# Optimization experiments

Hardware: AMD Instinct MI355X
Metric: run time of the kernel (lower is better)

Reference implementation:

```python
import jax, jax.numpy as jnp
import numpy as np

N_NODES = 50000
N_EDGES = 800000
N_FEAT = 64
HIDDEN = 64
N_GRAPHS = 64
N_CLASSES = 10
BN_EPS = 1e-5


def setup_inputs() -> dict:
    key = jax.random.key(0)
    ks = jax.random.split(key, 12)
    x = jax.random.normal(ks[0], (N_NODES, N_FEAT), dtype=jnp.float32)
    edge_index = jax.random.randint(ks[1], (2, N_EDGES), 0, N_NODES, dtype=jnp.int64)
    # equal-sized, sorted graph assignment so every graph is non-empty for max-pool
    batch = (jnp.arange(N_NODES, dtype=jnp.int64) * N_GRAPHS) // N_NODES
    s = 0.1
    return {
        "x": x,
        "edge_index": edge_index,
        "batch": batch,
        "W1": jax.random.normal(ks[2], (N_FEAT, HIDDEN), jnp.float32) * s,
        "b1": jnp.zeros((HIDDEN,), jnp.float32),
        "W2": jax.random.normal(ks[3], (HIDDEN, HIDDEN), jnp.float32) * s,
        "b2": jnp.zeros((HIDDEN,), jnp.float32),
        "W3": jax.random.normal(ks[4], (HIDDEN, HIDDEN), jnp.float32) * s,
        "b3": jnp.zeros((HIDDEN,), jnp.float32),
        # NOTE: source uses [Norm(hidden)]*3 -> ONE shared BatchNorm across layers
        "gamma": jnp.ones((HIDDEN,), jnp.float32),
        "beta": jnp.zeros((HIDDEN,), jnp.float32),
        "lin1_w": jax.random.normal(ks[5], (HIDDEN, HIDDEN), jnp.float32) * s,
        "lin1_b": jnp.zeros((HIDDEN,), jnp.float32),
        "lin2_w": jax.random.normal(ks[6], (HIDDEN, N_CLASSES), jnp.float32) * s,
        "lin2_b": jnp.zeros((N_CLASSES,), jnp.float32),
    }


def reference(x, edge_index, batch, W1, b1, W2, b2, W3, b3, gamma, beta,
              lin1_w, lin1_b, lin2_w, lin2_b):
    N = x.shape[0]
    src, dst = edge_index[0], edge_index[1]
    # GCN symmetric normalization with self-loops: deg = in-degree + 1
    deg = jax.ops.segment_sum(jnp.ones(src.shape[0], x.dtype), dst, num_segments=N) + 1.0
    dis = jax.lax.rsqrt(deg)                      # [N]
    coef = (dis[src] * dis[dst])[:, None]         # [E,1] edge norm
    self_coef = (dis * dis)[:, None]              # [N,1] self-loop norm

    def gcn_conv(h, W, b):
        h = h @ W                                  # [N,H] tiny GEMM
        agg = jax.ops.segment_sum(h[src] * coef, dst, num_segments=N)
        return agg + h * self_coef + b

    def batch_norm(h):
        mu = h.mean(axis=0)
        var = h.var(axis=0)                        # biased var, torch BN training mode
        return gamma * (h - mu) * jax.lax.rsqrt(var + BN_EPS) + beta

    out = x
    for W, b in ((W1, b1), (W2, b2), (W3, b3)):
        out = jax.nn.relu(batch_norm(gcn_conv(out, W, b)))

    emb = jax.ops.segment_max(out, batch, num_segments=N_GRAPHS)  # global_max_pool
    return jax.nn.relu(emb @ lin1_w + lin1_b) @ lin2_w + lin2_b
```

## Files before the change

kernel.cpp:

```cpp
#include <hip/hip_runtime.h>
#include <hip/hip_bf16.h>

#define N_NODES 50000
#define N_EDGES 800000
#define HID 64
#define N_GRAPHS 64
#define N_CLASSES 10
#define BN_EPS 1e-5f
#define NPART 196
#define FILL_BLOCKS 128

typedef unsigned int uint;
typedef unsigned short ushort;

__device__ __forceinline__ float blo(uint u) { return __uint_as_float(u << 16); }
__device__ __forceinline__ float bhi(uint u) { return __uint_as_float(u & 0xffff0000u); }
__device__ __forceinline__ unsigned short f2b(float f) {
  __hip_bfloat16 h = __float2bfloat16(f);
  return *reinterpret_cast<unsigned short*>(&h);
}


__global__ void k_count_deg(const int* __restrict__ dst, int* __restrict__ deg) {
  int e = blockIdx.x * blockDim.x + threadIdx.x;
  if (e < N_EDGES) atomicAdd(&deg[__builtin_nontemporal_load(&dst[e])], 1);
}

__global__ void k_scan_block(const int* __restrict__ deg, int* __restrict__ rowp,
                             int* __restrict__ bsum, float* __restrict__ dis) {
  __shared__ int s[256];
  int tid = threadIdx.x;
  int i = blockIdx.x * 256 + tid;
  int v = (i < N_NODES) ? deg[i] : 0;
  if (i < N_NODES) dis[i] = rsqrtf((float)v + 1.0f);
  s[tid] = v;
  __syncthreads();
  for (int off = 1; off < 256; off <<= 1) {
    int t = (tid >= off) ? s[tid - off] : 0;
    __syncthreads();
    s[tid] += t;
    __syncthreads();
  }
  if (i < N_NODES) rowp[i] = s[tid] - v;
  if (tid == 255) bsum[blockIdx.x] = s[255];
}

__global__ void k_scan_partials(int* __restrict__ bsum, int nb) {
  __shared__ int s[256];
  int tid = threadIdx.x;
  int v = (tid < nb) ? bsum[tid] : 0;
  s[tid] = v;
  __syncthreads();
  for (int off = 1; off < 256; off <<= 1) {
    int t = (tid >= off) ? s[tid - off] : 0;
    __syncthreads();
    s[tid] += t;
    __syncthreads();
  }
  if (tid < nb) bsum[tid] = s[tid] - v;
}

__global__ void k_scan_finish(int* __restrict__ rowp, const int* __restrict__ bsum,
                              int* __restrict__ pcur) {
  int i = blockIdx.x * blockDim.x + threadIdx.x;
  if (i < N_NODES) {
    int v = rowp[i] + bsum[i >> 8];
    rowp[i] = v;
    if ((i & 255) == 0) pcur[i >> 8] = v;
  }
  if (i == 0) rowp[N_NODES] = N_EDGES;
}

__global__ __launch_bounds__(256) void k_partA(const int* __restrict__ ei,
                                               int* __restrict__ pcur,
                                               uint* __restrict__ tmp) {
  __shared__ int lcnt[NPART];
  __shared__ int lbase[NPART];
  int tid = threadIdx.x;
  const int per = (N_EDGES + FILL_BLOCKS - 1) / FILL_BLOCKS;
  int c0 = blockIdx.x * per;
  int c1 = c0 + per;
  if (c1 > N_EDGES) c1 = N_EDGES;
  for (int i = tid; i < NPART; i += 256) lcnt[i] = 0;
  __syncthreads();
  for (int e = c0 + tid; e < c1; e += 256) {
    int d = __builtin_nontemporal_load(&ei[N_EDGES + e]);
    atomicAdd(&lcnt[d >> 8], 1);
  }
  __syncthreads();
  for (int p = tid; p < NPART; p += 256) lbase[p] = atomicAdd(&pcur[p], lcnt[p]);
  __syncthreads();
  for (int e = c0 + tid; e < c1; e += 256) {
    int s = __builtin_nontemporal_load(&ei[e]);
    int d = __builtin_nontemporal_load(&ei[N_EDGES + e]);
    int pos = atomicAdd(&lbase[d >> 8], 1);
    tmp[pos] = ((uint)s << 8) | (uint)(d & 255);
  }
}

__global__ __launch_bounds__(256) void k_partB(const uint* __restrict__ tmp,
                                               const int* __restrict__ rowp,
                                               const float* __restrict__ dis,
                                               uint* __restrict__ edata) {
  __shared__ int cur[256];
  __shared__ float sdis[256];
  int tid = threadIdx.x;
  int p = blockIdx.x;
  int n0 = p << 8;
  {
    int n = n0 + tid;
    cur[tid] = (n < N_NODES) ? rowp[n] : 0;
    sdis[tid] = (n < N_NODES) ? dis[n] : 0.f;
  }
  int base = rowp[n0];
  int endn = n0 + 256;
  if (endn > N_NODES) endn = N_NODES;
  int pend = rowp[endn];
  __syncthreads();
  for (int idx = base + tid; idx < pend; idx += 256) {
    uint t = __builtin_nontemporal_load(&tmp[idx]);
    uint s = t >> 8;
    uint dl = t & 255u;
    int pos = atomicAdd(&cur[dl], 1);
    float coef = dis[s] * sdis[dl];
    edata[pos] = (s << 16) | (uint)f2b(coef);
  }
}


template <bool IN_BF16>
__global__ __launch_bounds__(256) void k_gemm(const void* __restrict__ in,
                                              const float* __restrict__ W,
                                              __hip_bfloat16* __restrict__ out,
                                              float* __restrict__ stats_zero,
                                              const float* __restrict__ stats_in,
                                              const float* __restrict__ gamma,
                                              const float* __restrict__ beta) {
  __shared__ float Al[4][64];
  int tid = threadIdx.x;
  int wid = tid >> 6, f = tid & 63;
  if (blockIdx.x == 0) {
    for (int i = tid; i < 1024; i += 256) stats_zero[i] = 0.0f;
  }
  float Wreg[64];
#pragma unroll
  for (int k = 0; k < 64; ++k) Wreg[k] = W[k * 64 + f];
  float sc = 1.f, sh = 0.f;
  if (stats_in) {
    float s = 0.f, q = 0.f;
#pragma unroll
    for (int c = 0; c < 8; ++c) {
      s += stats_in[c * 128 + f];
      q += stats_in[c * 128 + 64 + f];
    }
    float mu = s * (1.0f / N_NODES);
    float var = q * (1.0f / N_NODES) - mu * mu;
    sc = gamma[f] * rsqrtf(var + BN_EPS);
    sh = beta[f] - mu * sc;
  }
  for (int n = blockIdx.x * 4 + wid; n < N_NODES; n += gridDim.x * 4) {
    float av;
    if (IN_BF16) {
      ushort u = ((const ushort*)in)[(n << 6) + f];
      av = __uint_as_float((uint)u << 16);
    } else {
      av = ((const float*)in)[(n << 6) + f];
    }
    if (stats_in) {
      av = fmaf(av, sc, sh);
      av = av > 0.f ? av : 0.f;
    }
    Al[wid][f] = av;
    float acc = 0.f;
    const float4* arow = (const float4*)Al[wid];
#pragma unroll
    for (int k4 = 0; k4 < 16; ++k4) {
      float4 a = arow[k4];
      acc = fmaf(a.x, Wreg[k4 * 4 + 0], acc);
      acc = fmaf(a.y, Wreg[k4 * 4 + 1], acc);
      acc = fmaf(a.z, Wreg[k4 * 4 + 2], acc);
      acc = fmaf(a.w, Wreg[k4 * 4 + 3], acc);
    }
    out[(n << 6) + f] = __float2bfloat16(acc);
  }
}

__global__ __launch_bounds__(256, 4) void k_agg_node(
    const __hip_bfloat16* __restrict__ hW, const float* __restrict__ dis,
    const int* __restrict__ rowp, const uint* __restrict__ edata,
    const float* __restrict__ bias, __hip_bfloat16* __restrict__ act,
    float* __restrict__ stats) {
  __shared__ float sstat[4][2][64];
  int tid = threadIdx.x;
  int wid = tid >> 6, lane = tid & 63;
  int g = lane >> 3, l8 = lane & 7;
  int n = (blockIdx.x * 4 + wid) * 8 + g;
  const uint4* hw4 = (const uint4*)hW;
  float pre[8] = {0, 0, 0, 0, 0, 0, 0, 0};
  float sq[8] = {0, 0, 0, 0, 0, 0, 0, 0};
  if (n < N_NODES) {
    int p0 = rowp[n], p1 = rowp[n + 1];
    float acc[8] = {0, 0, 0, 0, 0, 0, 0, 0};
    for (int pb = p0; pb < p1; pb += 8) {
      uint rec = (pb + l8 < p1) ? edata[pb + l8] : 0u;
      uint e[8];
#pragma unroll
      for (int u = 0; u < 8; ++u) e[u] = __shfl(rec, (g << 3) | u, 64);
#pragma unroll
      for (int h = 0; h < 2; ++h) {
        uint4 hv[4];
#pragma unroll
        for (int u = 0; u < 4; ++u) hv[u] = hw4[(e[h * 4 + u] >> 16) * 8 + l8];
#pragma unroll
        for (int u = 0; u < 4; ++u) {
          float wv = blo(e[h * 4 + u]);
          acc[0] = fmaf(blo(hv[u].x), wv, acc[0]);
          acc[1] = fmaf(bhi(hv[u].x), wv, acc[1]);
          acc[2] = fmaf(blo(hv[u].y), wv, acc[2]);
          acc[3] = fmaf(bhi(hv[u].y), wv, acc[3]);
          acc[4] = fmaf(blo(hv[u].z), wv, acc[4]);
          acc[5] = fmaf(bhi(hv[u].z), wv, acc[5]);
          acc[6] = fmaf(blo(hv[u].w), wv, acc[6]);
          acc[7] = fmaf(bhi(hv[u].w), wv, acc[7]);
        }
      }
    }
    float dn = dis[n];
    float dn2 = dn * dn;
    uint4 hs = hw4[n * 8 + l8];
    const float4* b4 = (const float4*)bias;
    float4 bA = b4[l8 * 2], bB = b4[l8 * 2 + 1];
    pre[0] = fmaf(blo(hs.x), dn2, acc[0]) + bA.x;
    pre[1] = fmaf(bhi(hs.x), dn2, acc[1]) + bA.y;
    pre[2] = fmaf(blo(hs.y), dn2, acc[2]) + bA.z;
    pre[3] = fmaf(bhi(hs.y), dn2, acc[3]) + bA.w;
    pre[4] = fmaf(blo(hs.z), dn2, acc[4]) + bB.x;
    pre[5] = fmaf(bhi(hs.z), dn2, acc[5]) + bB.y;
    pre[6] = fmaf(blo(hs.w), dn2, acc[6]) + bB.z;
    pre[7] = fmaf(bhi(hs.w), dn2, acc[7]) + bB.w;
    uint4 st;
    st.x = (uint)f2b(pre[0]) | ((uint)f2b(pre[1]) << 16);
    st.y = (uint)f2b(pre[2]) | ((uint)f2b(pre[3]) << 16);
    st.z = (uint)f2b(pre[4]) | ((uint)f2b(pre[5]) << 16);
    st.w = (uint)f2b(pre[6]) | ((uint)f2b(pre[7]) << 16);
    ((uint4*)act)[n * 8 + l8] = st;
#pragma unroll
    for (int i = 0; i < 8; ++i) sq[i] = pre[i] * pre[i];
  }
#pragma unroll
  for (int off = 8; off < 64; off <<= 1) {
#pragma unroll
    for (int i = 0; i < 8; ++i) {
      pre[i] += __shfl_xor(pre[i], off, 64);
      sq[i] += __shfl_xor(sq[i], off, 64);
    }
  }
  if (g == 0) {
#pragma unroll
    for (int i = 0; i < 8; ++i) {
      sstat[wid][0][l8 * 8 + i] = pre[i];
      sstat[wid][1][l8 * 8 + i] = sq[i];
    }
  }
  __syncthreads();
  if (tid < 128) {
    int which = tid >> 6, f = tid & 63;
    float s = sstat[0][which][f] + sstat[1][which][f] + sstat[2][which][f] +
              sstat[3][which][f];
    atomicAdd(&stats[(blockIdx.x & 7) * 128 + which * 64 + f], s);
  }
}


__global__ __launch_bounds__(256) void k_pool(const __hip_bfloat16* __restrict__ act,
                                              const float* __restrict__ stats_in,
                                              const float* __restrict__ gamma,
                                              const float* __restrict__ beta,
                                              float* __restrict__ pooled) {
  int g = blockIdx.x;
  int tid = threadIdx.x;
  int l16 = tid & 15;
  int r = tid >> 4;
  float sc[4], sh[4];
#pragma unroll
  for (int i = 0; i < 4; ++i) {
    int f = l16 * 4 + i;
    float s = 0.f, q = 0.f;
#pragma unroll
    for (int c = 0; c < 8; ++c) {
      s += stats_in[c * 128 + f];
      q += stats_in[c * 128 + 64 + f];
    }
    float mu = s * (1.0f / N_NODES);
    float var = q * (1.0f / N_NODES) - mu * mu;
    sc[i] = gamma[f] * rsqrtf(var + BN_EPS);
    sh[i] = beta[f] - mu * sc[i];
  }
  int gs = g * N_NODES;
  int start = (gs + 63) >> 6;
  int end = (gs + N_NODES + 63) >> 6;
  float m[4] = {0.f, 0.f, 0.f, 0.f};
  const uint2* a2 = (const uint2*)act;
  for (int n = start + r; n < end; n += 16) {
    uint2 v = a2[n * 16 + l16];
    m[0] = fmaxf(m[0], fmaf(blo(v.x), sc[0], sh[0]));
    m[1] = fmaxf(m[1], fmaf(bhi(v.x), sc[1], sh[1]));
    m[2] = fmaxf(m[2], fmaf(blo(v.y), sc[2], sh[2]));
    m[3] = fmaxf(m[3], fmaf(bhi(v.y), sc[3], sh[3]));
  }
  __shared__ float sm[16][64];
#pragma unroll
  for (int i = 0; i < 4; ++i) sm[r][l16 * 4 + i] = m[i];
  __syncthreads();
  if (tid < 64) {
    float mm = sm[0][tid];
#pragma unroll
    for (int rr = 1; rr < 16; ++rr) mm = fmaxf(mm, sm[rr][tid]);
    pooled[g * 64 + tid] = mm;
  }
}

__global__ __launch_bounds__(256) void k_final(const float* __restrict__ pooled,
                                               const float* __restrict__ w1,
                                               const float* __restrict__ b1,
                                               const float* __restrict__ w2,
                                               const float* __restrict__ b2,
                                               float* __restrict__ out) {
  __shared__ float P[64 * 64];
  __shared__ float Hd[64 * 64];
  int tid = threadIdx.x;
  for (int i = tid; i < 4096; i += 256) P[i] = pooled[i];
  __syncthreads();
  for (int i = tid; i < 4096; i += 256) {
    int g = i >> 6, j = i & 63;
    float acc = b1[j];
#pragma unroll
    for (int k = 0; k < 64; ++k) acc = fmaf(P[g * 64 + k], w1[k * 64 + j], acc);
    Hd[i] = acc > 0.f ? acc : 0.f;
  }
  __syncthreads();
  for (int i = tid; i < 640; i += 256) {
    int g = i / 10, c = i % 10;
    float acc = b2[c];
#pragma unroll
    for (int k = 0; k < 64; ++k) acc = fmaf(Hd[g * 64 + k], w2[k * 10 + c], acc);
    out[i] = acc;
  }
}


extern "C" void kernel_launch(void* const* d_in, const int* in_sizes, int n_in,
                              void* d_out, int out_size, void* d_ws, size_t ws_size,
                              hipStream_t stream) {
  const float* x = (const float*)d_in[0];
  const int* ei = (const int*)d_in[1];
  const float* W1 = (const float*)d_in[3];
  const float* b1 = (const float*)d_in[4];
  const float* W2 = (const float*)d_in[5];
  const float* b2 = (const float*)d_in[6];
  const float* W3 = (const float*)d_in[7];
  const float* b3 = (const float*)d_in[8];
  const float* gamma = (const float*)d_in[9];
  const float* beta = (const float*)d_in[10];
  const float* l1w = (const float*)d_in[11];
  const float* l1b = (const float*)d_in[12];
  const float* l2w = (const float*)d_in[13];
  const float* l2b = (const float*)d_in[14];
  float* out = (float*)d_out;

  char* ws = (char*)d_ws;
  size_t off = 0;
  auto alloc = [&](size_t bytes) {
    void* p = ws + off;
    off = (off + bytes + 255) & ~(size_t)255;
    return p;
  };
  int* deg = (int*)alloc(N_NODES * 4);
  int* rowp = (int*)alloc((N_NODES + 1) * 4);
  int* pcur = (int*)alloc(NPART * 4);
  int* bsum = (int*)alloc(256 * 4);
  uint* tmp = (uint*)alloc((size_t)N_EDGES * 4);
  uint* edata = (uint*)alloc((size_t)N_EDGES * 4);
  float* dis = (float*)alloc(N_NODES * 4);
  __hip_bfloat16* hW = (__hip_bfloat16*)alloc((size_t)N_NODES * 64 * 2);
  __hip_bfloat16* act = (__hip_bfloat16*)alloc((size_t)N_NODES * 64 * 2);
  float* statsL0 = (float*)alloc(1024 * 4);
  float* statsL1 = (float*)alloc(1024 * 4);
  float* statsL2 = (float*)alloc(1024 * 4);
  float* pooled = (float*)alloc(4096 * 4);

  int nsb = (N_NODES + 255) / 256;
  int nag = (N_NODES + 31) / 32;

  (void)hipMemsetAsync(deg, 0, N_NODES * 4, stream);
  k_count_deg<<<(N_EDGES + 255) / 256, 256, 0, stream>>>(ei + N_EDGES, deg);
  k_scan_block<<<nsb, 256, 0, stream>>>(deg, rowp, bsum, dis);
  k_scan_partials<<<1, 256, 0, stream>>>(bsum, nsb);
  k_scan_finish<<<nsb, 256, 0, stream>>>(rowp, bsum, pcur);
  k_partA<<<FILL_BLOCKS, 256, 0, stream>>>(ei, pcur, tmp);
  k_partB<<<NPART, 256, 0, stream>>>(tmp, rowp, dis, edata);

  k_gemm<false><<<2048, 256, 0, stream>>>(x, W1, hW, statsL0, nullptr, gamma, beta);
  k_agg_node<<<nag, 256, 0, stream>>>(hW, dis, rowp, edata, b1, act, statsL0);
  k_gemm<true><<<2048, 256, 0, stream>>>(act, W2, hW, statsL1, statsL0, gamma, beta);
  k_agg_node<<<nag, 256, 0, stream>>>(hW, dis, rowp, edata, b2, act, statsL1);
  k_gemm<true><<<2048, 256, 0, stream>>>(act, W3, hW, statsL2, statsL1, gamma, beta);
  k_agg_node<<<nag, 256, 0, stream>>>(hW, dis, rowp, edata, b3, act, statsL2);

  k_pool<<<N_GRAPHS, 256, 0, stream>>>(act, statsL2, gamma, beta, pooled);
  k_final<<<1, 256, 0, stream>>>(pooled, l1w, l1b, l2w, l2b, out);
}
```

Measured before the change: 227.0 us.

## Build CSR from partition histogram and store 16-bit source indices per edge

Replaces the per-node global-atomic degree count and three-kernel scan with a 196-bucket partition histogram and a single small scan. Per-node degrees, `dis` and `rowp` are now computed inside `k_partB` using shared-memory counting and a per-block scan. Each edge record shrinks from 4 bytes (16-bit source plus a bf16 coefficient) to a 2-byte source index. The aggregation kernel rebuilds the coefficient on the fly from `dis[src]*dis[dst]`. This cuts launch count, global atomic traffic and edge bandwidth, at the cost of an extra scattered `dis` load per edge in each of the three aggregation passes.

```diff
diff --git a/kernel.cpp b/kernel.cpp
--- a/kernel.cpp
+++ b/kernel.cpp
@@ -21,18 +21,33 @@
 }
 
 
-__global__ void k_count_deg(const int* __restrict__ dst, int* __restrict__ deg) {
-  int e = blockIdx.x * blockDim.x + threadIdx.x;
-  if (e < N_EDGES) atomicAdd(&deg[__builtin_nontemporal_load(&dst[e])], 1);
-}
-
-__global__ void k_scan_block(const int* __restrict__ deg, int* __restrict__ rowp,
-                             int* __restrict__ bsum, float* __restrict__ dis) {
+__global__ void k_zero_small(int* __restrict__ p, int n) {
+  int i = threadIdx.x;
+  if (i < n) p[i] = 0;
+}
+
+__global__ __launch_bounds__(256) void k_hist(const int* __restrict__ dst,
+                                              int* __restrict__ ghist) {
+  __shared__ int l[NPART];
+  int tid = threadIdx.x;
+  for (int i = tid; i < NPART; i += 256) l[i] = 0;
+  __syncthreads();
+  const int per = (N_EDGES + FILL_BLOCKS - 1) / FILL_BLOCKS;
+  int c0 = blockIdx.x * per;
+  int c1 = c0 + per;
+  if (c1 > N_EDGES) c1 = N_EDGES;
+  for (int e = c0 + tid; e < c1; e += 256)
+    atomicAdd(&l[__builtin_nontemporal_load(&dst[e]) >> 8], 1);
+  __syncthreads();
+  for (int p = tid; p < NPART; p += 256)
+    if (l[p]) atomicAdd(&ghist[p], l[p]);
+}
+
+__global__ void k_scan196(const int* __restrict__ ghist, int* __restrict__ bro,
+                          int* __restrict__ pcur, int* __restrict__ rowp) {
   __shared__ int s[256];
   int tid = threadIdx.x;
-  int i = blockIdx.x * 256 + tid;
-  int v = (i < N_NODES) ? deg[i] : 0;
-  if (i < N_NODES) dis[i] = rsqrtf((float)v + 1.0f);
+  int v = (tid < NPART) ? ghist[tid] : 0;
   s[tid] = v;
   __syncthreads();
   for (int off = 1; off < 256; off <<= 1) {
@@ -41,15 +56,64 @@
     s[tid] += t;
     __syncthreads();
   }
-  if (i < N_NODES) rowp[i] = s[tid] - v;
-  if (tid == 255) bsum[blockIdx.x] = s[255];
-}
-
-__global__ void k_scan_partials(int* __restrict__ bsum, int nb) {
+  if (tid < NPART) {
+    int e = s[tid] - v;
+    bro[tid] = e;
+    pcur[tid] = e;
+  }
+  if (tid == 0) {
+    bro[NPART] = N_EDGES;
+    rowp[N_NODES] = N_EDGES;
+  }
+}
+
+__global__ __launch_bounds__(256) void k_partA(const int* __restrict__ ei,
+                                               int* __restrict__ pcur,
+                                               uint* __restrict__ tmp) {
+  __shared__ int lcnt[NPART];
+  __shared__ int lbase[NPART];
+  int tid = threadIdx.x;
+  const int per = (N_EDGES + FILL_BLOCKS - 1) / FILL_BLOCKS;
+  int c0 = blockIdx.x * per;
+  int c1 = c0 + per;
+  if (c1 > N_EDGES) c1 = N_EDGES;
+  for (int i = tid; i < NPART; i += 256) lcnt[i] = 0;
+  __syncthreads();
+  for (int e = c0 + tid; e < c1; e += 256) {
+    int d = __builtin_nontemporal_load(&ei[N_EDGES + e]);
+    atomicAdd(&lcnt[d >> 8], 1);
+  }
+  __syncthreads();
+  for (int p = tid; p < NPART; p += 256) lbase[p] = atomicAdd(&pcur[p], lcnt[p]);
+  __syncthreads();
+  for (int e = c0 + tid; e < c1; e += 256) {
+    int s = __builtin_nontemporal_load(&ei[e]);
+    int d = __builtin_nontemporal_load(&ei[N_EDGES + e]);
+    int pos = atomicAdd(&lbase[d >> 8], 1);
+    tmp[pos] = ((uint)s << 8) | (uint)(d & 255);
+  }
+}
+
+__global__ __launch_bounds__(256) void k_partB(const uint* __restrict__ tmp,
+                                               const int* __restrict__ bro,
+                                               float* __restrict__ dis,
+                                               int* __restrict__ rowp,
+                                               ushort* __restrict__ eus) {
+  __shared__ int cnt[256];
   __shared__ int s[256];
-  int tid = threadIdx.x;
-  int v = (tid < nb) ? bsum[tid] : 0;
-  s[tid] = v;
+  __shared__ int cur[256];
+  int tid = threadIdx.x;
+  int p = blockIdx.x;
+  int base = bro[p], pend = bro[p + 1];
+  cnt[tid] = 0;
+  __syncthreads();
+  for (int idx = base + tid; idx < pend; idx += 256)
+    atomicAdd(&cnt[__builtin_nontemporal_load(&tmp[idx]) & 255u], 1);
+  __syncthreads();
+  int deg = cnt[tid];
+  int n = (p << 8) + tid;
+  if (n < N_NODES) dis[n] = rsqrtf((float)deg + 1.0f);
+  s[tid] = deg;
   __syncthreads();
   for (int off = 1; off < 256; off <<= 1) {
     int t = (tid >= off) ? s[tid - off] : 0;
@@ -57,73 +121,14 @@
     s[tid] += t;
     __syncthreads();
   }
-  if (tid < nb) bsum[tid] = s[tid] - v;
-}
-
-__global__ void k_scan_finish(int* __restrict__ rowp, const int* __restrict__ bsum,
-                              int* __restrict__ pcur) {
-  int i = blockIdx.x * blockDim.x + threadIdx.x;
-  if (i < N_NODES) {
-    int v = rowp[i] + bsum[i >> 8];
-    rowp[i] = v;
-    if ((i & 255) == 0) pcur[i >> 8] = v;
-  }
-  if (i == 0) rowp[N_NODES] = N_EDGES;
-}
-
-__global__ __launch_bounds__(256) void k_partA(const int* __restrict__ ei,
-                                               int* __restrict__ pcur,
-                                               uint* __restrict__ tmp) {
-  __shared__ int lcnt[NPART];
-  __shared__ int lbase[NPART];
-  int tid = threadIdx.x;
-  const int per = (N_EDGES + FILL_BLOCKS - 1) / FILL_BLOCKS;
-  int c0 = blockIdx.x * per;
-  int c1 = c0 + per;
-  if (c1 > N_EDGES) c1 = N_EDGES;
-  for (int i = tid; i < NPART; i += 256) lcnt[i] = 0;
-  __syncthreads();
-  for (int e = c0 + tid; e < c1; e += 256) {
-    int d = __builtin_nontemporal_load(&ei[N_EDGES + e]);
-    atomicAdd(&lcnt[d >> 8], 1);
-  }
-  __syncthreads();
-  for (int p = tid; p < NPART; p += 256) lbase[p] = atomicAdd(&pcur[p], lcnt[p]);
-  __syncthreads();
-  for (int e = c0 + tid; e < c1; e += 256) {
-    int s = __builtin_nontemporal_load(&ei[e]);
-    int d = __builtin_nontemporal_load(&ei[N_EDGES + e]);
-    int pos = atomicAdd(&lbase[d >> 8], 1);
-    tmp[pos] = ((uint)s << 8) | (uint)(d & 255);
-  }
-}
-
-__global__ __launch_bounds__(256) void k_partB(const uint* __restrict__ tmp,
-                                               const int* __restrict__ rowp,
-                                               const float* __restrict__ dis,
-                                               uint* __restrict__ edata) {
-  __shared__ int cur[256];
-  __shared__ float sdis[256];
-  int tid = threadIdx.x;
-  int p = blockIdx.x;
-  int n0 = p << 8;
-  {
-    int n = n0 + tid;
-    cur[tid] = (n < N_NODES) ? rowp[n] : 0;
-    sdis[tid] = (n < N_NODES) ? dis[n] : 0.f;
-  }
-  int base = rowp[n0];
-  int endn = n0 + 256;
-  if (endn > N_NODES) endn = N_NODES;
-  int pend = rowp[endn];
+  int start = base + s[tid] - deg;
+  if (n < N_NODES) rowp[n] = start;
+  cur[tid] = start;
   __syncthreads();
   for (int idx = base + tid; idx < pend; idx += 256) {
     uint t = __builtin_nontemporal_load(&tmp[idx]);
-    uint s = t >> 8;
-    uint dl = t & 255u;
-    int pos = atomicAdd(&cur[dl], 1);
-    float coef = dis[s] * sdis[dl];
-    edata[pos] = (s << 16) | (uint)f2b(coef);
+    int pos = atomicAdd(&cur[t & 255u], 1);
+    eus[pos] = (ushort)(t >> 8);
   }
 }
 
@@ -187,7 +192,7 @@
 
 __global__ __launch_bounds__(256, 4) void k_agg_node(
     const __hip_bfloat16* __restrict__ hW, const float* __restrict__ dis,
-    const int* __restrict__ rowp, const uint* __restrict__ edata,
+    const int* __restrict__ rowp, const ushort* __restrict__ eus,
     const float* __restrict__ bias, __hip_bfloat16* __restrict__ act,
     float* __restrict__ stats) {
   __shared__ float sstat[4][2][64];
@@ -200,20 +205,27 @@
   float sq[8] = {0, 0, 0, 0, 0, 0, 0, 0};
   if (n < N_NODES) {
     int p0 = rowp[n], p1 = rowp[n + 1];
+    float dn = dis[n];
     float acc[8] = {0, 0, 0, 0, 0, 0, 0, 0};
     for (int pb = p0; pb < p1; pb += 8) {
-      uint rec = (pb + l8 < p1) ? edata[pb + l8] : 0u;
-      uint e[8];
-#pragma unroll
-      for (int u = 0; u < 8; ++u) e[u] = __shfl(rec, (g << 3) | u, 64);
+      int idx = pb + l8;
+      if (idx >= N_EDGES) idx = N_EDGES - 1;
+      uint rs = eus[idx];
 #pragma unroll
       for (int h = 0; h < 2; ++h) {
+        uint e4[4];
+        float ds4[4];
         uint4 hv[4];
 #pragma unroll
-        for (int u = 0; u < 4; ++u) hv[u] = hw4[(e[h * 4 + u] >> 16) * 8 + l8];
+        for (int u = 0; u < 4; ++u) e4[u] = __shfl(rs, (g << 3) | (h * 4 + u), 64);
 #pragma unroll
         for (int u = 0; u < 4; ++u) {
-          float wv = blo(e[h * 4 + u]);
+          hv[u] = hw4[e4[u] * 8 + l8];
+          ds4[u] = dis[e4[u]];
+        }
+#pragma unroll
+        for (int u = 0; u < 4; ++u) {
+          float wv = (pb + h * 4 + u < p1) ? ds4[u] * dn : 0.f;
           acc[0] = fmaf(blo(hv[u].x), wv, acc[0]);
           acc[1] = fmaf(bhi(hv[u].x), wv, acc[1]);
           acc[2] = fmaf(blo(hv[u].y), wv, acc[2]);
@@ -225,7 +237,6 @@
         }
       }
     }
-    float dn = dis[n];
     float dn2 = dn * dn;
     uint4 hs = hw4[n * 8 + l8];
     const float4* b4 = (const float4*)bias;
@@ -375,12 +386,12 @@
     off = (off + bytes + 255) & ~(size_t)255;
     return p;
   };
-  int* deg = (int*)alloc(N_NODES * 4);
+  int* ghist = (int*)alloc(NPART * 4);
+  int* bro = (int*)alloc((NPART + 1) * 4);
+  int* pcur = (int*)alloc(NPART * 4);
   int* rowp = (int*)alloc((N_NODES + 1) * 4);
-  int* pcur = (int*)alloc(NPART * 4);
-  int* bsum = (int*)alloc(256 * 4);
   uint* tmp = (uint*)alloc((size_t)N_EDGES * 4);
-  uint* edata = (uint*)alloc((size_t)N_EDGES * 4);
+  ushort* eus = (ushort*)alloc((size_t)N_EDGES * 2 + 512);
   float* dis = (float*)alloc(N_NODES * 4);
   __hip_bfloat16* hW = (__hip_bfloat16*)alloc((size_t)N_NODES * 64 * 2);
   __hip_bfloat16* act = (__hip_bfloat16*)alloc((size_t)N_NODES * 64 * 2);
@@ -389,23 +400,20 @@
   float* statsL2 = (float*)alloc(1024 * 4);
   float* pooled = (float*)alloc(4096 * 4);
 
-  int nsb = (N_NODES + 255) / 256;
   int nag = (N_NODES + 31) / 32;
 
-  (void)hipMemsetAsync(deg, 0, N_NODES * 4, stream);
-  k_count_deg<<<(N_EDGES + 255) / 256, 256, 0, stream>>>(ei + N_EDGES, deg);
-  k_scan_block<<<nsb, 256, 0, stream>>>(deg, rowp, bsum, dis);
-  k_scan_partials<<<1, 256, 0, stream>>>(bsum, nsb);
-  k_scan_finish<<<nsb, 256, 0, stream>>>(rowp, bsum, pcur);
+  k_zero_small<<<1, 256, 0, stream>>>(ghist, NPART);
+  k_hist<<<FILL_BLOCKS, 256, 0, stream>>>(ei + N_EDGES, ghist);
+  k_scan196<<<1, 256, 0, stream>>>(ghist, bro, pcur, rowp);
   k_partA<<<FILL_BLOCKS, 256, 0, stream>>>(ei, pcur, tmp);
-  k_partB<<<NPART, 256, 0, stream>>>(tmp, rowp, dis, edata);
+  k_partB<<<NPART, 256, 0, stream>>>(tmp, bro, dis, rowp, eus);
 
   k_gemm<false><<<2048, 256, 0, stream>>>(x, W1, hW, statsL0, nullptr, gamma, beta);
-  k_agg_node<<<nag, 256, 0, stream>>>(hW, dis, rowp, edata, b1, act, statsL0);
+  k_agg_node<<<nag, 256, 0, stream>>>(hW, dis, rowp, eus, b1, act, statsL0);
   k_gemm<true><<<2048, 256, 0, stream>>>(act, W2, hW, statsL1, statsL0, gamma, beta);
-  k_agg_node<<<nag, 256, 0, stream>>>(hW, dis, rowp, edata, b2, act, statsL1);
+  k_agg_node<<<nag, 256, 0, stream>>>(hW, dis, rowp, eus, b2, act, statsL1);
   k_gemm<true><<<2048, 256, 0, stream>>>(act, W3, hW, statsL2, statsL1, gamma, beta);
-  k_agg_node<<<nag, 256, 0, stream>>>(hW, dis, rowp, edata, b3, act, statsL2);
+  k_agg_node<<<nag, 256, 0, stream>>>(hW, dis, rowp, eus, b3, act, statsL2);
 
   k_pool<<<N_GRAPHS, 256, 0, stream>>>(act, statsL2, gamma, beta, pooled);
   k_final<<<1, 256, 0, stream>>>(pooled, l1w, l1b, l2w, l2b, out);
```

New measurement: 201.6 us. 1.13x faster.
